# Kernel tuning notes

Measured on AMD Instinct MI355X. Metric: run time of the kernel, lower is better.

## Reference

```python
import jax, jax.numpy as jnp
import numpy as np

N_NODES = 50000
N_EDGES = 800000
FEATURES = 64
HIDDEN = 128
OUT_DIM = 64
CUTOFF = 10.0
STEP = 0.1
N_MU = 100  # len(arange(0, 10, 0.1))


def setup_inputs() -> dict:
    key = jax.random.key(0)
    k_h, k_src, k_dst, k_norm, k_w1, k_w2 = jax.random.split(key, 6)
    h = jax.random.normal(k_h, (N_NODES, FEATURES), dtype=jnp.float32)
    src = jax.random.randint(k_src, (N_EDGES,), 0, N_NODES, dtype=jnp.int64)
    dst = jax.random.randint(k_dst, (N_EDGES,), 0, N_NODES, dtype=jnp.int64)
    edge_norm = jax.random.uniform(k_norm, (N_EDGES,), dtype=jnp.float32) * CUTOFF
    mu = jnp.arange(0.0, CUTOFF, STEP, dtype=jnp.float32)  # [100], learned param
    in_dim = 2 * FEATURES + N_MU
    # xavier_normal with gain split across 2 linear layers: layer_gain = 1.0
    s1 = float(np.sqrt(2.0 / (in_dim + HIDDEN)))
    s2 = float(np.sqrt(2.0 / (HIDDEN + OUT_DIM)))
    W1 = jax.random.normal(k_w1, (HIDDEN, in_dim), dtype=jnp.float32) * s1
    W2 = jax.random.normal(k_w2, (OUT_DIM, HIDDEN), dtype=jnp.float32) * s2
    return {"h": h, "src": src, "dst": dst, "edge_norm": edge_norm,
            "mu": mu, "W1": W1, "W2": W2}


def reference(h, src, dst, edge_norm, mu, W1, W2):
    # Gaussian RBF expansion of edge distances: [E, n_mu]
    d_emb = jnp.exp((-1.0 / STEP) * (mu[None, :] - edge_norm[:, None]) ** 2)
    # gather endpoint features and concat: [E, 2*features + n_mu]
    x = jnp.concatenate((h[src], h[dst], d_emb), axis=-1)
    # MLP: Linear(no bias) -> SiLU -> Linear(no bias)
    hdn = jax.nn.silu(x @ W1.T)
    return hdn @ W2.T
```

## Files before the change

### kernel.cpp

```cpp
#include <hip/hip_runtime.h>
#include <hip/hip_bf16.h>


#define FEAT     64
#define NMU      100
#define K1_REAL  228
#define HID      128
#define ODIM     64
#define K2       128
#define WEDGES   32
#define NWAVES   8
#define BEDGES   (WEDGES * NWAVES)
#define LDH2     136
#define HN8      400000

typedef __bf16 bf16x8 __attribute__((ext_vector_type(8)));
typedef float  fx4    __attribute__((ext_vector_type(4)));

__global__ void pack_w(const float* __restrict__ W1, const float* __restrict__ W2,
                       __bf16* __restrict__ B1, __bf16* __restrict__ B2) {
    int i = blockIdx.x * 256 + threadIdx.x;
    if (i < 32768) {
        int j  = i & 7;
        int n  = (i >> 3) & 127;
        int qk = i >> 10;
        int k  = (qk >> 2) * 32 + (qk & 3) * 8 + j;
        float v = (k < K1_REAL) ? W1[n * K1_REAL + k] : 0.0f;
        B1[i] = (__bf16)v;
    } else {
        int t = i - 32768;
        int j  = t & 7;
        int n  = (t >> 3) & 63;
        int qk = t >> 9;
        int k  = (qk >> 2) * 32 + (qk & 3) * 8 + j;
        B2[t] = (__bf16)W2[n * K2 + k];
    }
}

__global__ void pack_h(const float* __restrict__ h, __bf16* __restrict__ hb) {
    int i = blockIdx.x * 256 + threadIdx.x;
    if (i >= HN8) return;
    const float4* p = (const float4*)h + (size_t)i * 2;
    float4 v0 = p[0];
    float4 v1 = p[1];
    bf16x8 b = { (__bf16)v0.x, (__bf16)v0.y, (__bf16)v0.z, (__bf16)v0.w,
                 (__bf16)v1.x, (__bf16)v1.y, (__bf16)v1.z, (__bf16)v1.w };
    ((bf16x8*)hb)[i] = b;
}

__device__ __forceinline__ bf16x8 hfrag_f32(const float* __restrict__ h, int node, int cb) {
    const float4* p = (const float4*)(h + (size_t)node * FEAT + cb);
    float4 v0 = p[0];
    float4 v1 = p[1];
    bf16x8 a = { (__bf16)v0.x, (__bf16)v0.y, (__bf16)v0.z, (__bf16)v0.w,
                 (__bf16)v1.x, (__bf16)v1.y, (__bf16)v1.z, (__bf16)v1.w };
    return a;
}

template<bool HB16>
__global__ __launch_bounds__(512, 2)
void edges_fused(const float* __restrict__ h,
                 const __bf16* __restrict__ hb,
                 const int*   __restrict__ src,
                 const int*   __restrict__ dst,
                 const float* __restrict__ enorm,
                 const float* __restrict__ mu,
                 const __bf16* __restrict__ B1,
                 const __bf16* __restrict__ B2,
                 float* __restrict__ out) {
    __shared__ __bf16 B1s[32768];
    __shared__ __bf16 B2s[8192];
    __shared__ __bf16 Hs[NWAVES * WEDGES * LDH2];

    const int tid  = threadIdx.x;
    const int w    = tid >> 6;
    const int lane = tid & 63;
    const int ln   = lane & 15;
    const int q    = lane >> 4;
    const int g0   = blockIdx.x * BEDGES + w * WEDGES;

    int nsrc[2], ndst[2];
    float dval[2];
#pragma unroll
    for (int mt = 0; mt < 2; ++mt) {
        int e = g0 + mt * 16 + ln;
        nsrc[mt] = src[e];
        ndst[mt] = dst[e];
        dval[mt] = enorm[e];
    }

    bf16x8 ag[4][2];
#pragma unroll
    for (int kk = 0; kk < 4; ++kk) {
        const int cb = (kk & 1) * 32 + q * 8;
#pragma unroll
        for (int mt = 0; mt < 2; ++mt) {
            int node = (kk < 2) ? nsrc[mt] : ndst[mt];
            if constexpr (HB16)
                ag[kk][mt] = *(const bf16x8*)(hb + (size_t)node * FEAT + cb);
            else
                ag[kk][mt] = hfrag_f32(h, node, cb);
        }
    }

    {
        const bf16x8* gB1 = (const bf16x8*)B1;
        const bf16x8* gB2 = (const bf16x8*)B2;
        bf16x8* sB1 = (bf16x8*)B1s;
        bf16x8* sB2 = (bf16x8*)B2s;
#pragma unroll
        for (int it = 0; it < 8; ++it) {
            int g = it * 512 + tid;
            sB1[g] = gB1[g];
        }
#pragma unroll
        for (int it = 0; it < 2; ++it) {
            int g = it * 512 + tid;
            sB2[g] = gB2[g];
        }
    }
    __syncthreads();

    fx4 acc1[2][8];
#pragma unroll
    for (int mt = 0; mt < 2; ++mt)
#pragma unroll
        for (int nt = 0; nt < 8; ++nt)
            acc1[mt][nt] = (fx4){0.f, 0.f, 0.f, 0.f};

#pragma unroll
    for (int kk = 0; kk < 4; ++kk) {
#pragma unroll
        for (int nt = 0; nt < 8; ++nt) {
            bf16x8 b = *(const bf16x8*)&B1s[(((kk * 4 + q) * 128) + nt * 16 + ln) * 8];
            acc1[0][nt] = __builtin_amdgcn_mfma_f32_16x16x32_bf16(ag[kk][0], b, acc1[0][nt], 0, 0, 0);
            acc1[1][nt] = __builtin_amdgcn_mfma_f32_16x16x32_bf16(ag[kk][1], b, acc1[1][nt], 0, 0, 0);
        }
    }

#pragma unroll
    for (int kk = 4; kk < 7; ++kk) {
        const int c0 = (kk - 4) * 32 + q * 8;
        float4 m0 = *(const float4*)(mu + c0);
        float4 m1 = *(const float4*)(mu + c0 + 4);
        bf16x8 a[2];
#pragma unroll
        for (int mt = 0; mt < 2; ++mt) {
            float d = dval[mt];
            float t0 = m0.x - d, t1 = m0.y - d, t2 = m0.z - d, t3 = m0.w - d;
            float t4 = m1.x - d, t5 = m1.y - d, t6 = m1.z - d, t7 = m1.w - d;
            a[mt] = (bf16x8){ (__bf16)__expf(-10.f * t0 * t0), (__bf16)__expf(-10.f * t1 * t1),
                              (__bf16)__expf(-10.f * t2 * t2), (__bf16)__expf(-10.f * t3 * t3),
                              (__bf16)__expf(-10.f * t4 * t4), (__bf16)__expf(-10.f * t5 * t5),
                              (__bf16)__expf(-10.f * t6 * t6), (__bf16)__expf(-10.f * t7 * t7) };
        }
#pragma unroll
        for (int nt = 0; nt < 8; ++nt) {
            bf16x8 b = *(const bf16x8*)&B1s[(((kk * 4 + q) * 128) + nt * 16 + ln) * 8];
            acc1[0][nt] = __builtin_amdgcn_mfma_f32_16x16x32_bf16(a[0], b, acc1[0][nt], 0, 0, 0);
            acc1[1][nt] = __builtin_amdgcn_mfma_f32_16x16x32_bf16(a[1], b, acc1[1][nt], 0, 0, 0);
        }
    }

    {
        float4 m7 = *(const float4*)(mu + 96);
        const __bf16 zz = (__bf16)0.0f;
        const bool qz = (q == 0);
        bf16x8 a[2];
#pragma unroll
        for (int mt = 0; mt < 2; ++mt) {
            float d = dval[mt];
            float t0 = m7.x - d, t1 = m7.y - d, t2 = m7.z - d, t3 = m7.w - d;
            a[mt] = (bf16x8){ qz ? (__bf16)__expf(-10.f * t0 * t0) : zz,
                              qz ? (__bf16)__expf(-10.f * t1 * t1) : zz,
                              qz ? (__bf16)__expf(-10.f * t2 * t2) : zz,
                              qz ? (__bf16)__expf(-10.f * t3 * t3) : zz,
                              zz, zz, zz, zz };
        }
#pragma unroll
        for (int nt = 0; nt < 8; ++nt) {
            bf16x8 b = *(const bf16x8*)&B1s[(((7 * 4 + q) * 128) + nt * 16 + ln) * 8];
            acc1[0][nt] = __builtin_amdgcn_mfma_f32_16x16x32_bf16(a[0], b, acc1[0][nt], 0, 0, 0);
            acc1[1][nt] = __builtin_amdgcn_mfma_f32_16x16x32_bf16(a[1], b, acc1[1][nt], 0, 0, 0);
        }
    }

    __bf16* Hw = &Hs[w * WEDGES * LDH2];
#pragma unroll
    for (int mt = 0; mt < 2; ++mt)
#pragma unroll
        for (int nt = 0; nt < 8; ++nt)
#pragma unroll
            for (int r = 0; r < 4; ++r) {
                float z = acc1[mt][nt][r];
                float s = z * __builtin_amdgcn_rcpf(1.0f + __expf(-z));
                Hw[(mt * 16 + q * 4 + r) * LDH2 + nt * 16 + ln] = (__bf16)s;
            }

    fx4 acc2[2][4];
#pragma unroll
    for (int mt = 0; mt < 2; ++mt)
#pragma unroll
        for (int nt = 0; nt < 4; ++nt)
            acc2[mt][nt] = (fx4){0.f, 0.f, 0.f, 0.f};

#pragma unroll
    for (int kk = 0; kk < 4; ++kk) {
        bf16x8 a2[2];
#pragma unroll
        for (int mt = 0; mt < 2; ++mt)
            a2[mt] = *(const bf16x8*)&Hw[(mt * 16 + ln) * LDH2 + kk * 32 + q * 8];
#pragma unroll
        for (int nt = 0; nt < 4; ++nt) {
            bf16x8 b2 = *(const bf16x8*)&B2s[(((kk * 4 + q) * 64) + nt * 16 + ln) * 8];
            acc2[0][nt] = __builtin_amdgcn_mfma_f32_16x16x32_bf16(a2[0], b2, acc2[0][nt], 0, 0, 0);
            acc2[1][nt] = __builtin_amdgcn_mfma_f32_16x16x32_bf16(a2[1], b2, acc2[1][nt], 0, 0, 0);
        }
    }

#pragma unroll
    for (int mt = 0; mt < 2; ++mt)
#pragma unroll
        for (int nt = 0; nt < 4; ++nt)
#pragma unroll
            for (int r = 0; r < 4; ++r)
                out[(size_t)(g0 + mt * 16 + q * 4 + r) * ODIM + nt * 16 + ln] = acc2[mt][nt][r];
}

extern "C" void kernel_launch(void* const* d_in, const int* in_sizes, int n_in,
                              void* d_out, int out_size, void* d_ws, size_t ws_size,
                              hipStream_t stream) {
    const float* h   = (const float*)d_in[0];
    const int*   src = (const int*)d_in[1];
    const int*   dst = (const int*)d_in[2];
    const float* en  = (const float*)d_in[3];
    const float* mu  = (const float*)d_in[4];
    const float* W1  = (const float*)d_in[5];
    const float* W2  = (const float*)d_in[6];

    __bf16* B1 = (__bf16*)d_ws;
    __bf16* B2 = (__bf16*)((char*)d_ws + 65536);
    __bf16* HB = (__bf16*)((char*)d_ws + 81920);

    const size_t ws_needed = 81920 + (size_t)HN8 * 8 * sizeof(__bf16);
    const bool   use_hb    = ws_size >= ws_needed;

    pack_w<<<160, 256, 0, stream>>>(W1, W2, B1, B2);

    const int E = in_sizes[1];
    const int nblocks = E / BEDGES;

    if (use_hb) {
        pack_h<<<(HN8 + 255) / 256, 256, 0, stream>>>(h, HB);
        edges_fused<true><<<nblocks, 512, 0, stream>>>(h, HB, src, dst, en, mu, B1, B2, (float*)d_out);
    } else {
        edges_fused<false><<<nblocks, 512, 0, stream>>>(h, nullptr, src, dst, en, mu, B1, B2, (float*)d_out);
    }
}
```

Before: 328.2 us.

## Make edge kernel persistent with software-pipelined gather of next chunk

Replaces one-block-per-256-edges launch with a fixed grid of 256 persistent blocks whose waves loop over 32-edge chunks. Weights are staged into LDS once per block instead of once per 256 edges. The next chunk's indices are loaded and its node features gathered while the current chunk's GEMMs run, hiding gather latency. Risks include higher register pressure from the extra prefetch buffers, and a 256-block grid with 2 blocks per CU may not fill all CUs.

After: 446.4 us. +36.0%, slower.

```diff
diff --git a/kernel.cpp b/kernel.cpp
--- a/kernel.cpp
+++ b/kernel.cpp
@@ -10,9 +10,9 @@
 #define K2       128
 #define WEDGES   32
 #define NWAVES   8
-#define BEDGES   (WEDGES * NWAVES)
 #define LDH2     136
 #define HN8      400000
+#define GRID     256
 
 typedef __bf16 bf16x8 __attribute__((ext_vector_type(8)));
 typedef float  fx4    __attribute__((ext_vector_type(4)));
@@ -67,7 +67,8 @@
                  const float* __restrict__ mu,
                  const __bf16* __restrict__ B1,
                  const __bf16* __restrict__ B2,
-                 float* __restrict__ out) {
+                 float* __restrict__ out,
+                 int nchunk) {
     __shared__ __bf16 B1s[32768];
     __shared__ __bf16 B2s[8192];
     __shared__ __bf16 Hs[NWAVES * WEDGES * LDH2];
@@ -77,30 +78,18 @@
     const int lane = tid & 63;
     const int ln   = lane & 15;
     const int q    = lane >> 4;
-    const int g0   = blockIdx.x * BEDGES + w * WEDGES;
-
-    int nsrc[2], ndst[2];
-    float dval[2];
+    const int wid  = blockIdx.x * NWAVES + w;
+    const int NW   = gridDim.x * NWAVES;
+
+    int c = wid;
+    int nsA[2], ndA[2];
+    float dvA[2];
 #pragma unroll
     for (int mt = 0; mt < 2; ++mt) {
-        int e = g0 + mt * 16 + ln;
-        nsrc[mt] = src[e];
-        ndst[mt] = dst[e];
-        dval[mt] = enorm[e];
-    }
-
-    bf16x8 ag[4][2];
-#pragma unroll
-    for (int kk = 0; kk < 4; ++kk) {
-        const int cb = (kk & 1) * 32 + q * 8;
-#pragma unroll
-        for (int mt = 0; mt < 2; ++mt) {
-            int node = (kk < 2) ? nsrc[mt] : ndst[mt];
-            if constexpr (HB16)
-                ag[kk][mt] = *(const bf16x8*)(hb + (size_t)node * FEAT + cb);
-            else
-                ag[kk][mt] = hfrag_f32(h, node, cb);
-        }
+        int e = c * WEDGES + mt * 16 + ln;
+        nsA[mt] = src[e];
+        ndA[mt] = dst[e];
+        dvA[mt] = enorm[e];
     }
 
     {
@@ -119,112 +108,163 @@
             sB2[g] = gB2[g];
         }
     }
+
+    bf16x8 ag[4][2];
+#pragma unroll
+    for (int kk = 0; kk < 4; ++kk) {
+        const int cb = (kk & 1) * 32 + q * 8;
+#pragma unroll
+        for (int mt = 0; mt < 2; ++mt) {
+            int node = (kk < 2) ? nsA[mt] : ndA[mt];
+            if constexpr (HB16)
+                ag[kk][mt] = *(const bf16x8*)(hb + (size_t)node * FEAT + cb);
+            else
+                ag[kk][mt] = hfrag_f32(h, node, cb);
+        }
+    }
+
     __syncthreads();
 
-    fx4 acc1[2][8];
-#pragma unroll
-    for (int mt = 0; mt < 2; ++mt)
-#pragma unroll
-        for (int nt = 0; nt < 8; ++nt)
-            acc1[mt][nt] = (fx4){0.f, 0.f, 0.f, 0.f};
-
-#pragma unroll
-    for (int kk = 0; kk < 4; ++kk) {
-#pragma unroll
-        for (int nt = 0; nt < 8; ++nt) {
-            bf16x8 b = *(const bf16x8*)&B1s[(((kk * 4 + q) * 128) + nt * 16 + ln) * 8];
-            acc1[0][nt] = __builtin_amdgcn_mfma_f32_16x16x32_bf16(ag[kk][0], b, acc1[0][nt], 0, 0, 0);
-            acc1[1][nt] = __builtin_amdgcn_mfma_f32_16x16x32_bf16(ag[kk][1], b, acc1[1][nt], 0, 0, 0);
-        }
-    }
-
-#pragma unroll
-    for (int kk = 4; kk < 7; ++kk) {
-        const int c0 = (kk - 4) * 32 + q * 8;
-        float4 m0 = *(const float4*)(mu + c0);
-        float4 m1 = *(const float4*)(mu + c0 + 4);
-        bf16x8 a[2];
-#pragma unroll
-        for (int mt = 0; mt < 2; ++mt) {
-            float d = dval[mt];
-            float t0 = m0.x - d, t1 = m0.y - d, t2 = m0.z - d, t3 = m0.w - d;
-            float t4 = m1.x - d, t5 = m1.y - d, t6 = m1.z - d, t7 = m1.w - d;
-            a[mt] = (bf16x8){ (__bf16)__expf(-10.f * t0 * t0), (__bf16)__expf(-10.f * t1 * t1),
-                              (__bf16)__expf(-10.f * t2 * t2), (__bf16)__expf(-10.f * t3 * t3),
-                              (__bf16)__expf(-10.f * t4 * t4), (__bf16)__expf(-10.f * t5 * t5),
-                              (__bf16)__expf(-10.f * t6 * t6), (__bf16)__expf(-10.f * t7 * t7) };
-        }
-#pragma unroll
-        for (int nt = 0; nt < 8; ++nt) {
-            bf16x8 b = *(const bf16x8*)&B1s[(((kk * 4 + q) * 128) + nt * 16 + ln) * 8];
-            acc1[0][nt] = __builtin_amdgcn_mfma_f32_16x16x32_bf16(a[0], b, acc1[0][nt], 0, 0, 0);
-            acc1[1][nt] = __builtin_amdgcn_mfma_f32_16x16x32_bf16(a[1], b, acc1[1][nt], 0, 0, 0);
-        }
-    }
-
-    {
-        float4 m7 = *(const float4*)(mu + 96);
-        const __bf16 zz = (__bf16)0.0f;
-        const bool qz = (q == 0);
-        bf16x8 a[2];
-#pragma unroll
-        for (int mt = 0; mt < 2; ++mt) {
-            float d = dval[mt];
-            float t0 = m7.x - d, t1 = m7.y - d, t2 = m7.z - d, t3 = m7.w - d;
-            a[mt] = (bf16x8){ qz ? (__bf16)__expf(-10.f * t0 * t0) : zz,
-                              qz ? (__bf16)__expf(-10.f * t1 * t1) : zz,
-                              qz ? (__bf16)__expf(-10.f * t2 * t2) : zz,
-                              qz ? (__bf16)__expf(-10.f * t3 * t3) : zz,
-                              zz, zz, zz, zz };
-        }
-#pragma unroll
-        for (int nt = 0; nt < 8; ++nt) {
-            bf16x8 b = *(const bf16x8*)&B1s[(((7 * 4 + q) * 128) + nt * 16 + ln) * 8];
-            acc1[0][nt] = __builtin_amdgcn_mfma_f32_16x16x32_bf16(a[0], b, acc1[0][nt], 0, 0, 0);
-            acc1[1][nt] = __builtin_amdgcn_mfma_f32_16x16x32_bf16(a[1], b, acc1[1][nt], 0, 0, 0);
-        }
-    }
-
     __bf16* Hw = &Hs[w * WEDGES * LDH2];
-#pragma unroll
-    for (int mt = 0; mt < 2; ++mt)
-#pragma unroll
-        for (int nt = 0; nt < 8; ++nt)
-#pragma unroll
-            for (int r = 0; r < 4; ++r) {
-                float z = acc1[mt][nt][r];
-                float s = z * __builtin_amdgcn_rcpf(1.0f + __expf(-z));
-                Hw[(mt * 16 + q * 4 + r) * LDH2 + nt * 16 + ln] = (__bf16)s;
-            }
-
-    fx4 acc2[2][4];
-#pragma unroll
-    for (int mt = 0; mt < 2; ++mt)
-#pragma unroll
-        for (int nt = 0; nt < 4; ++nt)
-            acc2[mt][nt] = (fx4){0.f, 0.f, 0.f, 0.f};
-
-#pragma unroll
-    for (int kk = 0; kk < 4; ++kk) {
-        bf16x8 a2[2];
-#pragma unroll
-        for (int mt = 0; mt < 2; ++mt)
-            a2[mt] = *(const bf16x8*)&Hw[(mt * 16 + ln) * LDH2 + kk * 32 + q * 8];
-#pragma unroll
-        for (int nt = 0; nt < 4; ++nt) {
-            bf16x8 b2 = *(const bf16x8*)&B2s[(((kk * 4 + q) * 64) + nt * 16 + ln) * 8];
-            acc2[0][nt] = __builtin_amdgcn_mfma_f32_16x16x32_bf16(a2[0], b2, acc2[0][nt], 0, 0, 0);
-            acc2[1][nt] = __builtin_amdgcn_mfma_f32_16x16x32_bf16(a2[1], b2, acc2[1][nt], 0, 0, 0);
-        }
-    }
-
-#pragma unroll
-    for (int mt = 0; mt < 2; ++mt)
-#pragma unroll
-        for (int nt = 0; nt < 4; ++nt)
-#pragma unroll
-            for (int r = 0; r < 4; ++r)
-                out[(size_t)(g0 + mt * 16 + q * 4 + r) * ODIM + nt * 16 + ln] = acc2[mt][nt][r];
+
+    while (c < nchunk) {
+        const int cn = c + NW;
+        const bool haveN = (cn < nchunk);
+
+        int nsB[2], ndB[2];
+        float dvB[2];
+        if (haveN) {
+#pragma unroll
+            for (int mt = 0; mt < 2; ++mt) {
+                int e = cn * WEDGES + mt * 16 + ln;
+                nsB[mt] = src[e];
+                ndB[mt] = dst[e];
+                dvB[mt] = enorm[e];
+            }
+        }
+
+        fx4 acc1[2][8];
+#pragma unroll
+        for (int mt = 0; mt < 2; ++mt)
+#pragma unroll
+            for (int nt = 0; nt < 8; ++nt)
+                acc1[mt][nt] = (fx4){0.f, 0.f, 0.f, 0.f};
+
+#pragma unroll
+        for (int kk = 4; kk < 7; ++kk) {
+            const int c0 = (kk - 4) * 32 + q * 8;
+            float4 m0 = *(const float4*)(mu + c0);
+            float4 m1 = *(const float4*)(mu + c0 + 4);
+            bf16x8 a[2];
+#pragma unroll
+            for (int mt = 0; mt < 2; ++mt) {
+                float d = dvA[mt];
+                float t0 = m0.x - d, t1 = m0.y - d, t2 = m0.z - d, t3 = m0.w - d;
+                float t4 = m1.x - d, t5 = m1.y - d, t6 = m1.z - d, t7 = m1.w - d;
+                a[mt] = (bf16x8){ (__bf16)__expf(-10.f * t0 * t0), (__bf16)__expf(-10.f * t1 * t1),
+                                  (__bf16)__expf(-10.f * t2 * t2), (__bf16)__expf(-10.f * t3 * t3),
+                                  (__bf16)__expf(-10.f * t4 * t4), (__bf16)__expf(-10.f * t5 * t5),
+                                  (__bf16)__expf(-10.f * t6 * t6), (__bf16)__expf(-10.f * t7 * t7) };
+            }
+#pragma unroll
+            for (int nt = 0; nt < 8; ++nt) {
+                bf16x8 b = *(const bf16x8*)&B1s[(((kk * 4 + q) * 128) + nt * 16 + ln) * 8];
+                acc1[0][nt] = __builtin_amdgcn_mfma_f32_16x16x32_bf16(a[0], b, acc1[0][nt], 0, 0, 0);
+                acc1[1][nt] = __builtin_amdgcn_mfma_f32_16x16x32_bf16(a[1], b, acc1[1][nt], 0, 0, 0);
+            }
+        }
+        {
+            float4 m7 = *(const float4*)(mu + 96);
+            const __bf16 zz = (__bf16)0.0f;
+            const bool qz = (q == 0);
+            bf16x8 a[2];
+#pragma unroll
+            for (int mt = 0; mt < 2; ++mt) {
+                float d = dvA[mt];
+                float t0 = m7.x - d, t1 = m7.y - d, t2 = m7.z - d, t3 = m7.w - d;
+                a[mt] = (bf16x8){ qz ? (__bf16)__expf(-10.f * t0 * t0) : zz,
+                                  qz ? (__bf16)__expf(-10.f * t1 * t1) : zz,
+                                  qz ? (__bf16)__expf(-10.f * t2 * t2) : zz,
+                                  qz ? (__bf16)__expf(-10.f * t3 * t3) : zz,
+                                  zz, zz, zz, zz };
+            }
+#pragma unroll
+            for (int nt = 0; nt < 8; ++nt) {
+                bf16x8 b = *(const bf16x8*)&B1s[(((7 * 4 + q) * 128) + nt * 16 + ln) * 8];
+                acc1[0][nt] = __builtin_amdgcn_mfma_f32_16x16x32_bf16(a[0], b, acc1[0][nt], 0, 0, 0);
+                acc1[1][nt] = __builtin_amdgcn_mfma_f32_16x16x32_bf16(a[1], b, acc1[1][nt], 0, 0, 0);
+            }
+        }
+#pragma unroll
+        for (int kk = 0; kk < 4; ++kk) {
+#pragma unroll
+            for (int nt = 0; nt < 8; ++nt) {
+                bf16x8 b = *(const bf16x8*)&B1s[(((kk * 4 + q) * 128) + nt * 16 + ln) * 8];
+                acc1[0][nt] = __builtin_amdgcn_mfma_f32_16x16x32_bf16(ag[kk][0], b, acc1[0][nt], 0, 0, 0);
+                acc1[1][nt] = __builtin_amdgcn_mfma_f32_16x16x32_bf16(ag[kk][1], b, acc1[1][nt], 0, 0, 0);
+            }
+        }
+
+        if (haveN) {
+#pragma unroll
+            for (int kk = 0; kk < 4; ++kk) {
+                const int cb = (kk & 1) * 32 + q * 8;
+#pragma unroll
+                for (int mt = 0; mt < 2; ++mt) {
+                    int node = (kk < 2) ? nsB[mt] : ndB[mt];
+                    if constexpr (HB16)
+                        ag[kk][mt] = *(const bf16x8*)(hb + (size_t)node * FEAT + cb);
+                    else
+                        ag[kk][mt] = hfrag_f32(h, node, cb);
+                }
+            }
+        }
+
+#pragma unroll
+        for (int mt = 0; mt < 2; ++mt)
+#pragma unroll
+            for (int nt = 0; nt < 8; ++nt)
+#pragma unroll
+                for (int r = 0; r < 4; ++r) {
+                    float z = acc1[mt][nt][r];
+                    float s = z * __builtin_amdgcn_rcpf(1.0f + __expf(-z));
+                    Hw[(mt * 16 + q * 4 + r) * LDH2 + nt * 16 + ln] = (__bf16)s;
+                }
+
+        fx4 acc2[2][4];
+#pragma unroll
+        for (int mt = 0; mt < 2; ++mt)
+#pragma unroll
+            for (int nt = 0; nt < 4; ++nt)
+                acc2[mt][nt] = (fx4){0.f, 0.f, 0.f, 0.f};
+
+#pragma unroll
+        for (int kk = 0; kk < 4; ++kk) {
+            bf16x8 a2[2];
+#pragma unroll
+            for (int mt = 0; mt < 2; ++mt)
+                a2[mt] = *(const bf16x8*)&Hw[(mt * 16 + ln) * LDH2 + kk * 32 + q * 8];
+#pragma unroll
+            for (int nt = 0; nt < 4; ++nt) {
+                bf16x8 b2 = *(const bf16x8*)&B2s[(((kk * 4 + q) * 64) + nt * 16 + ln) * 8];
+                acc2[0][nt] = __builtin_amdgcn_mfma_f32_16x16x32_bf16(a2[0], b2, acc2[0][nt], 0, 0, 0);
+                acc2[1][nt] = __builtin_amdgcn_mfma_f32_16x16x32_bf16(a2[1], b2, acc2[1][nt], 0, 0, 0);
+            }
+        }
+
+        const int g0 = c * WEDGES;
+#pragma unroll
+        for (int mt = 0; mt < 2; ++mt)
+#pragma unroll
+            for (int nt = 0; nt < 4; ++nt)
+#pragma unroll
+                for (int r = 0; r < 4; ++r)
+                    out[(size_t)(g0 + mt * 16 + q * 4 + r) * ODIM + nt * 16 + ln] = acc2[mt][nt][r];
+
+        dvA[0] = dvB[0];
+        dvA[1] = dvB[1];
+        c = cn;
+    }
 }
 
 extern "C" void kernel_launch(void* const* d_in, const int* in_sizes, int n_in,
@@ -248,12 +288,12 @@
     pack_w<<<160, 256, 0, stream>>>(W1, W2, B1, B2);
 
     const int E = in_sizes[1];
-    const int nblocks = E / BEDGES;
+    const int nchunk = E / WEDGES;
 
     if (use_hb) {
         pack_h<<<(HN8 + 255) / 256, 256, 0, stream>>>(h, HB);
-        edges_fused<true><<<nblocks, 512, 0, stream>>>(h, HB, src, dst, en, mu, B1, B2, (float*)d_out);
+        edges_fused<true><<<GRID, 512, 0, stream>>>(h, HB, src, dst, en, mu, B1, B2, (float*)d_out, nchunk);
     } else {
-        edges_fused<false><<<nblocks, 512, 0, stream>>>(h, nullptr, src, dst, en, mu, B1, B2, (float*)d_out);
-    }
-}
+        edges_fused<false><<<GRID, 512, 0, stream>>>(h, nullptr, src, dst, en, mu, B1, B2, (float*)d_out, nchunk);
+    }
+}
```

## Double block size, halve per-wave H staging, and reorder gather-dependent MFMAs last

Applied to the files above, without the earlier changes.

Blocks grow from 512 to 1024 threads (16 waves), so the LDS copy of the packed weights is amortized over twice as many edges. The per-wave hidden-activation buffer shrinks to 16 rows by running the second GEMM one 16-edge tile at a time, which saves LDS and accumulator registers. The RBF-part MFMAs now run before the gathered-feature MFMAs, to hide gather latency. It also adds a partial-block guard. Risks are register pressure under the tighter launch bounds and barrier stalls across more waves.

After: 324.4 us. Within noise of the previous version (-1.2%).

```diff
diff --git a/kernel.cpp b/kernel.cpp
--- a/kernel.cpp
+++ b/kernel.cpp
@@ -9,9 +9,10 @@
 #define ODIM     64
 #define K2       128
 #define WEDGES   32
-#define NWAVES   8
+#define NWAVES   16
 #define BEDGES   (WEDGES * NWAVES)
 #define LDH2     136
+#define HROWS    16
 #define HN8      400000
 
 typedef __bf16 bf16x8 __attribute__((ext_vector_type(8)));
@@ -58,7 +59,7 @@
 }
 
 template<bool HB16>
-__global__ __launch_bounds__(512, 2)
+__global__ __launch_bounds__(1024, 4)
 void edges_fused(const float* __restrict__ h,
                  const __bf16* __restrict__ hb,
                  const int*   __restrict__ src,
@@ -67,10 +68,11 @@
                  const float* __restrict__ mu,
                  const __bf16* __restrict__ B1,
                  const __bf16* __restrict__ B2,
-                 float* __restrict__ out) {
+                 float* __restrict__ out,
+                 int E) {
     __shared__ __bf16 B1s[32768];
     __shared__ __bf16 B2s[8192];
-    __shared__ __bf16 Hs[NWAVES * WEDGES * LDH2];
+    __shared__ __bf16 Hs[NWAVES * HROWS * LDH2];
 
     const int tid  = threadIdx.x;
     const int w    = tid >> 6;
@@ -78,28 +80,30 @@
     const int ln   = lane & 15;
     const int q    = lane >> 4;
     const int g0   = blockIdx.x * BEDGES + w * WEDGES;
+    const bool act = (g0 < E);
 
     int nsrc[2], ndst[2];
     float dval[2];
-#pragma unroll
-    for (int mt = 0; mt < 2; ++mt) {
-        int e = g0 + mt * 16 + ln;
-        nsrc[mt] = src[e];
-        ndst[mt] = dst[e];
-        dval[mt] = enorm[e];
-    }
-
     bf16x8 ag[4][2];
-#pragma unroll
-    for (int kk = 0; kk < 4; ++kk) {
-        const int cb = (kk & 1) * 32 + q * 8;
+    if (act) {
 #pragma unroll
         for (int mt = 0; mt < 2; ++mt) {
-            int node = (kk < 2) ? nsrc[mt] : ndst[mt];
-            if constexpr (HB16)
-                ag[kk][mt] = *(const bf16x8*)(hb + (size_t)node * FEAT + cb);
-            else
-                ag[kk][mt] = hfrag_f32(h, node, cb);
+            int e = g0 + mt * 16 + ln;
+            nsrc[mt] = src[e];
+            ndst[mt] = dst[e];
+            dval[mt] = enorm[e];
+        }
+#pragma unroll
+        for (int kk = 0; kk < 4; ++kk) {
+            const int cb = (kk & 1) * 32 + q * 8;
+#pragma unroll
+            for (int mt = 0; mt < 2; ++mt) {
+                int node = (kk < 2) ? nsrc[mt] : ndst[mt];
+                if constexpr (HB16)
+                    ag[kk][mt] = *(const bf16x8*)(hb + (size_t)node * FEAT + cb);
+                else
+                    ag[kk][mt] = hfrag_f32(h, node, cb);
+            }
         }
     }
 
@@ -109,17 +113,14 @@
         bf16x8* sB1 = (bf16x8*)B1s;
         bf16x8* sB2 = (bf16x8*)B2s;
 #pragma unroll
-        for (int it = 0; it < 8; ++it) {
-            int g = it * 512 + tid;
+        for (int it = 0; it < 4; ++it) {
+            int g = it * 1024 + tid;
             sB1[g] = gB1[g];
         }
-#pragma unroll
-        for (int it = 0; it < 2; ++it) {
-            int g = it * 512 + tid;
-            sB2[g] = gB2[g];
-        }
+        sB2[tid] = gB2[tid];
     }
     __syncthreads();
+    if (!act) return;
 
     fx4 acc1[2][8];
 #pragma unroll
@@ -127,16 +128,6 @@
 #pragma unroll
         for (int nt = 0; nt < 8; ++nt)
             acc1[mt][nt] = (fx4){0.f, 0.f, 0.f, 0.f};
-
-#pragma unroll
-    for (int kk = 0; kk < 4; ++kk) {
-#pragma unroll
-        for (int nt = 0; nt < 8; ++nt) {
-            bf16x8 b = *(const bf16x8*)&B1s[(((kk * 4 + q) * 128) + nt * 16 + ln) * 8];
-            acc1[0][nt] = __builtin_amdgcn_mfma_f32_16x16x32_bf16(ag[kk][0], b, acc1[0][nt], 0, 0, 0);
-            acc1[1][nt] = __builtin_amdgcn_mfma_f32_16x16x32_bf16(ag[kk][1], b, acc1[1][nt], 0, 0, 0);
-        }
-    }
 
 #pragma unroll
     for (int kk = 4; kk < 7; ++kk) {
@@ -161,7 +152,6 @@
             acc1[1][nt] = __builtin_amdgcn_mfma_f32_16x16x32_bf16(a[1], b, acc1[1][nt], 0, 0, 0);
         }
     }
-
     {
         float4 m7 = *(const float4*)(mu + 96);
         const __bf16 zz = (__bf16)0.0f;
@@ -184,47 +174,48 @@
             acc1[1][nt] = __builtin_amdgcn_mfma_f32_16x16x32_bf16(a[1], b, acc1[1][nt], 0, 0, 0);
         }
     }
-
-    __bf16* Hw = &Hs[w * WEDGES * LDH2];
-#pragma unroll
-    for (int mt = 0; mt < 2; ++mt)
+#pragma unroll
+    for (int kk = 0; kk < 4; ++kk) {
+#pragma unroll
+        for (int nt = 0; nt < 8; ++nt) {
+            bf16x8 b = *(const bf16x8*)&B1s[(((kk * 4 + q) * 128) + nt * 16 + ln) * 8];
+            acc1[0][nt] = __builtin_amdgcn_mfma_f32_16x16x32_bf16(ag[kk][0], b, acc1[0][nt], 0, 0, 0);
+            acc1[1][nt] = __builtin_amdgcn_mfma_f32_16x16x32_bf16(ag[kk][1], b, acc1[1][nt], 0, 0, 0);
+        }
+    }
+
+    __bf16* Hw = &Hs[w * HROWS * LDH2];
+#pragma unroll
+    for (int mt = 0; mt < 2; ++mt) {
 #pragma unroll
         for (int nt = 0; nt < 8; ++nt)
 #pragma unroll
             for (int r = 0; r < 4; ++r) {
                 float z = acc1[mt][nt][r];
                 float s = z * __builtin_amdgcn_rcpf(1.0f + __expf(-z));
-                Hw[(mt * 16 + q * 4 + r) * LDH2 + nt * 16 + ln] = (__bf16)s;
+                Hw[(q * 4 + r) * LDH2 + nt * 16 + ln] = (__bf16)s;
             }
 
-    fx4 acc2[2][4];
-#pragma unroll
-    for (int mt = 0; mt < 2; ++mt)
+        fx4 acc2[4];
 #pragma unroll
         for (int nt = 0; nt < 4; ++nt)
-            acc2[mt][nt] = (fx4){0.f, 0.f, 0.f, 0.f};
-
-#pragma unroll
-    for (int kk = 0; kk < 4; ++kk) {
-        bf16x8 a2[2];
-#pragma unroll
-        for (int mt = 0; mt < 2; ++mt)
-            a2[mt] = *(const bf16x8*)&Hw[(mt * 16 + ln) * LDH2 + kk * 32 + q * 8];
-#pragma unroll
-        for (int nt = 0; nt < 4; ++nt) {
-            bf16x8 b2 = *(const bf16x8*)&B2s[(((kk * 4 + q) * 64) + nt * 16 + ln) * 8];
-            acc2[0][nt] = __builtin_amdgcn_mfma_f32_16x16x32_bf16(a2[0], b2, acc2[0][nt], 0, 0, 0);
-            acc2[1][nt] = __builtin_amdgcn_mfma_f32_16x16x32_bf16(a2[1], b2, acc2[1][nt], 0, 0, 0);
-        }
-    }
-
-#pragma unroll
-    for (int mt = 0; mt < 2; ++mt)
+            acc2[nt] = (fx4){0.f, 0.f, 0.f, 0.f};
+#pragma unroll
+        for (int kk = 0; kk < 4; ++kk) {
+            bf16x8 a2 = *(const bf16x8*)&Hw[ln * LDH2 + kk * 32 + q * 8];
+#pragma unroll
+            for (int nt = 0; nt < 4; ++nt) {
+                bf16x8 b2 = *(const bf16x8*)&B2s[(((kk * 4 + q) * 64) + nt * 16 + ln) * 8];
+                acc2[nt] = __builtin_amdgcn_mfma_f32_16x16x32_bf16(a2, b2, acc2[nt], 0, 0, 0);
+            }
+        }
+
 #pragma unroll
         for (int nt = 0; nt < 4; ++nt)
 #pragma unroll
             for (int r = 0; r < 4; ++r)
-                out[(size_t)(g0 + mt * 16 + q * 4 + r) * ODIM + nt * 16 + ln] = acc2[mt][nt][r];
+                out[(size_t)(g0 + mt * 16 + q * 4 + r) * ODIM + nt * 16 + ln] = acc2[nt][r];
+    }
 }
 
 extern "C" void kernel_launch(void* const* d_in, const int* in_sizes, int n_in,
@@ -248,12 +239,12 @@
     pack_w<<<160, 256, 0, stream>>>(W1, W2, B1, B2);
 
     const int E = in_sizes[1];
-    const int nblocks = E / BEDGES;
+    const int nblocks = (E + BEDGES - 1) / BEDGES;
 
     if (use_hb) {
         pack_h<<<(HN8 + 255) / 256, 256, 0, stream>>>(h, HB);
-        edges_fused<true><<<nblocks, 512, 0, stream>>>(h, HB, src, dst, en, mu, B1, B2, (float*)d_out);
+        edges_fused<true><<<nblocks, 1024, 0, stream>>>(h, HB, src, dst, en, mu, B1, B2, (float*)d_out, E);
     } else {
-        edges_fused<false><<<nblocks, 512, 0, stream>>>(h, nullptr, src, dst, en, mu, B1, B2, (float*)d_out);
-    }
-}
+        edges_fused<false><<<nblocks, 1024, 0, stream>>>(h, nullptr, src, dst, en, mu, B1, B2, (float*)d_out, E);
+    }
+}
```
